# Kernel tuning notes

Hardware: AMD Instinct MI355X
Metric: run time of the kernel (lower is better)

Reference implementation:

```python
import jax, jax.numpy as jnp
import numpy as np

D_MODEL = 1024
EXPAND = 2
D_INNER = D_MODEL * EXPAND  # 2048 independent SSM channels
D_STATE = 16
BATCH = 4
SEQ = 4096


def setup_inputs() -> dict:
    key = jax.random.key(0)
    ks = jax.random.split(key, 10)
    w = lambda k, shape, scale=0.02: jax.random.normal(k, shape, jnp.float32) * scale
    return {
        "x": jax.random.normal(ks[0], (BATCH, SEQ, D_MODEL), jnp.float32),
        "w_in": w(ks[1], (D_MODEL, D_INNER)),
        "b_in": jnp.zeros((D_INNER,), jnp.float32),
        "w_gate": w(ks[2], (D_MODEL, D_INNER)),
        "b_gate": jnp.zeros((D_INNER,), jnp.float32),
        # per-channel linear SSM params: h_t = A h_{t-1} + B x_t ; y_t = C . h_t
        "A": w(ks[3], (D_INNER, D_STATE, D_STATE), 0.05),  # small spectral radius -> stable recurrence
        "B_ssm": w(ks[4], (D_INNER, D_STATE), 0.1),
        "C_ssm": w(ks[5], (D_INNER, D_STATE), 0.1),
        "w_out": w(ks[6], (D_INNER, D_MODEL)),
        "b_out": jnp.zeros((D_MODEL,), jnp.float32),
    }


def reference(x, w_in, b_in, w_gate, b_gate, A, B_ssm, C_ssm, w_out, b_out):
    # x: [B, S, D]
    x_proj = x @ w_in + b_in                     # [B, S, C]
    gate = jax.nn.sigmoid(x @ w_gate + b_gate)   # [B, S, C]

    def step(h, xt):
        # h: [B, C, N] state for all channels; xt: [B, C] scalar input per channel
        h = jnp.einsum("cnm,bcm->bcn", A, h) + B_ssm[None] * xt[:, :, None]
        y = jnp.einsum("bcn,cn->bc", h, C_ssm)
        return h, y

    h0 = jnp.zeros((x.shape[0], D_INNER, D_STATE), x.dtype)
    xs = jnp.swapaxes(x_proj, 0, 1)              # [S, B, C]
    _, ys = jax.lax.scan(step, h0, xs)           # ys: [S, B, C]
    ssm_out = jnp.swapaxes(ys, 0, 1)             # [B, S, C]

    y = ssm_out * gate
    return y @ w_out + b_out                     # [B, S, D]
```

## Files before the change

kernel.cpp:

```cpp
#include <hip/hip_runtime.h>
#include <hip/hip_bf16.h>

#define D_MODEL 1024
#define D_INNER 2048
#define D_STATE 16
#define BATCH   4
#define SEQ     4096
#define MROWS   (BATCH * SEQ)

#define LTAPS 16
#define TSPAN 64

using bf16 = __hip_bfloat16;

typedef __attribute__((ext_vector_type(8))) short bf16x8;
typedef __attribute__((ext_vector_type(4))) float f32x4;

__device__ __forceinline__ float bf2f(bf16 v) { return __bfloat162float(v); }
__device__ __forceinline__ unsigned short f2bfbits(float f) {
  bf16 h = __float2bfloat16(f);
  return *(unsigned short*)&h;
}

#define AS1CAST(p) ((const __attribute__((address_space(1))) unsigned int*)(unsigned long long)(p))
#define AS3CAST(p) ((__attribute__((address_space(3))) unsigned int*)(unsigned long long)(p))

#define FENCE() asm volatile("" ::: "memory")
#define BAR() do { FENCE(); __builtin_amdgcn_s_barrier(); FENCE(); } while (0)
#define WAIT_LGKM0() asm volatile("s_waitcnt lgkmcnt(0)" ::: "memory")

#define TILE_E (256 * 64)

struct G8 {
  const bf16 *gA, *gB;
  size_t K64, K128;
  int stageLds;
  int baseA0, baseA1;
  int baseB0, baseB1;
  int wr, wc, lane;
};

__device__ __forceinline__ void g8_setup(G8& g, const bf16* A, const bf16* BT,
                                         int m0, int n0, int K)
{
  const int tid = threadIdx.x;
  g.lane = tid & 63;
  const int wv = tid >> 6;
  g.wr = wv >> 2;
  g.wc = wv & 3;
  const int lr = g.lane >> 3, sl = g.lane & 7;
  g.gA = A  + (size_t)(m0 + wv * 8 + lr) * K + (sl ^ lr) * 8;
  g.gB = BT + (size_t)(n0 + wv * 8 + lr) * K + (sl ^ lr) * 8;
  g.K64  = (size_t)64 * K;
  g.K128 = (size_t)128 * K;
  g.stageLds = wv * 8 * 64;
  const int fla = g.lane & 15, cb = g.lane >> 4;
  const int s0 = cb ^ (fla & 7), s1 = s0 ^ 4;
  g.baseA0 = (g.wr * 64 + fla) * 64 + s0 * 8;
  g.baseA1 = (g.wr * 64 + fla) * 64 + s1 * 8;
  g.baseB0 = (g.wc * 32 + fla) * 64 + s0 * 8;
  g.baseB1 = (g.wc * 32 + fla) * 64 + s1 * 8;
}

__device__ __forceinline__ void g8_stageA(const G8& g, bf16* dstTile, int h, int tau)
{
  const bf16* s = g.gA + (h ? g.K128 : (size_t)0) + (size_t)tau * 64;
  bf16* d = dstTile + g.stageLds + h * (128 * 64);
  __builtin_amdgcn_global_load_lds(AS1CAST(s), AS3CAST(d), 16, 0, 0);
  __builtin_amdgcn_global_load_lds(AS1CAST(s + g.K64), AS3CAST(d + 64 * 64), 16, 0, 0);
}

__device__ __forceinline__ void g8_stageB(const G8& g, bf16* dstTile, int h, int tau)
{
  const bf16* s = g.gB + (h ? g.K128 : (size_t)0) + (size_t)tau * 64;
  bf16* d = dstTile + g.stageLds + h * (128 * 64);
  __builtin_amdgcn_global_load_lds(AS1CAST(s), AS3CAST(d), 16, 0, 0);
  __builtin_amdgcn_global_load_lds(AS1CAST(s + g.K64), AS3CAST(d + 64 * 64), 16, 0, 0);
}

#define LOAD_A(MH) do { _Pragma("unroll") \
  for (int mi = 0; mi < 4; ++mi) { \
    af[mi][0] = *(const bf16x8*)&At[g.baseA0 + (MH) * 8192 + mi * 1024]; \
    af[mi][1] = *(const bf16x8*)&At[g.baseA1 + (MH) * 8192 + mi * 1024]; \
  } } while (0)

#define LOAD_B(NH) do { _Pragma("unroll") \
  for (int ni = 0; ni < 2; ++ni) { \
    bfr[ni][0] = *(const bf16x8*)&Bt[g.baseB0 + (NH) * 8192 + ni * 1024]; \
    bfr[ni][1] = *(const bf16x8*)&Bt[g.baseB1 + (NH) * 8192 + ni * 1024]; \
  } } while (0)

#define MFMA_Q(MH, NH) do { _Pragma("unroll") \
  for (int mi = 0; mi < 4; ++mi) { _Pragma("unroll") \
    for (int ni = 0; ni < 2; ++ni) { \
      acc[MH][NH][mi][ni] = __builtin_amdgcn_mfma_f32_16x16x32_bf16( \
          af[mi][0], bfr[ni][0], acc[MH][NH][mi][ni], 0, 0, 0); \
      acc[MH][NH][mi][ni] = __builtin_amdgcn_mfma_f32_16x16x32_bf16( \
          af[mi][1], bfr[ni][1], acc[MH][NH][mi][ni], 0, 0, 0); \
    } } } while (0)

__device__ __forceinline__ void g8_main(const G8& g, bf16* As, bf16* Bs,
                                        f32x4 (&acc)[2][2][4][2], int K)
{
  const int nt = K >> 6;
  bf16* A0 = As;  bf16* A1 = As + TILE_E;
  bf16* B0 = Bs;  bf16* B1 = Bs + TILE_E;

  g8_stageA(g, A0, 0, 0);
  g8_stageB(g, B0, 1, 0);
  g8_stageA(g, A0, 1, 0);
  g8_stageB(g, B0, 0, 0);
  if (nt > 1) {
    g8_stageA(g, A1, 0, 1);
    g8_stageB(g, B1, 1, 1);
    g8_stageA(g, A1, 1, 1);
    asm volatile("s_waitcnt vmcnt(6)" ::: "memory");
  } else {
    asm volatile("s_waitcnt vmcnt(0)" ::: "memory");
  }
  BAR();

  bf16x8 af[4][2], bfr[2][2];

  for (int t = 0; t < nt; ++t) {
    const bf16* At = (t & 1) ? A1 : A0;
    const bf16* Bt = (t & 1) ? B1 : B0;
    bf16* Asame = (t & 1) ? A1 : A0;
    bf16* Bsame = (t & 1) ? B1 : B0;
    bf16* Bnext = (t & 1) ? B0 : B1;

    LOAD_A(0); LOAD_B(0);
    if (t + 1 < nt) g8_stageB(g, Bnext, 0, t + 1);
    asm volatile("s_waitcnt lgkmcnt(8)" ::: "memory");
    BAR();
    WAIT_LGKM0();
    __builtin_amdgcn_s_setprio(1);
    MFMA_Q(0, 0);
    __builtin_amdgcn_s_setprio(0);
    BAR();

    LOAD_B(1);
    if (t + 2 < nt) g8_stageA(g, Asame, 0, t + 2);
    BAR();
    WAIT_LGKM0();
    __builtin_amdgcn_s_setprio(1);
    MFMA_Q(0, 1);
    __builtin_amdgcn_s_setprio(0);
    BAR();

    LOAD_A(1);
    if (t + 2 < nt) g8_stageB(g, Bsame, 1, t + 2);
    BAR();
    WAIT_LGKM0();
    __builtin_amdgcn_s_setprio(1);
    MFMA_Q(1, 1);
    __builtin_amdgcn_s_setprio(0);
    BAR();

    LOAD_B(0);
    if (t + 2 < nt) g8_stageA(g, Asame, 1, t + 2);
    if (t < nt - 2) asm volatile("s_waitcnt vmcnt(6)" ::: "memory");
    else            asm volatile("s_waitcnt vmcnt(0)" ::: "memory");
    BAR();
    WAIT_LGKM0();
    __builtin_amdgcn_s_setprio(1);
    MFMA_Q(1, 0);
    __builtin_amdgcn_s_setprio(0);
    BAR();
  }
}

__global__ __launch_bounds__(512, 2) void gemm_proj_dual(
    const bf16* __restrict__ A,
    const bf16* __restrict__ BT,
    const float* __restrict__ bias_in, const float* __restrict__ bias_gate,
    bf16* __restrict__ xp, bf16* __restrict__ gate)
{
  __shared__ alignas(16) bf16 As[2 * TILE_E];
  __shared__ alignas(16) bf16 Bs[2 * TILE_E];

  const int b = blockIdx.x;
  const int swz = (b & 7) * 128 + (b >> 3);
  const int bm = swz >> 4, bn = swz & 15;
  const int m0 = bm * 256, n0 = bn * 256;

  G8 g;
  g8_setup(g, A, BT, m0, n0, D_MODEL);

  f32x4 acc[2][2][4][2];
#pragma unroll
  for (int a1 = 0; a1 < 2; ++a1)
#pragma unroll
    for (int a2 = 0; a2 < 2; ++a2)
#pragma unroll
      for (int a3 = 0; a3 < 4; ++a3)
#pragma unroll
        for (int a4 = 0; a4 < 2; ++a4)
          acc[a1][a2][a3][a4] = (f32x4){0.f, 0.f, 0.f, 0.f};

  g8_main(g, As, Bs, acc, D_MODEL);

  const bool isGate = (n0 >= D_INNER);
  const int  nloc0  = n0 - (isGate ? D_INNER : 0);
  const float* bias = isGate ? bias_gate : bias_in;
  bf16* dst         = isGate ? gate : xp;

  const int crow = (g.lane >> 4) * 4;
  const int ccol = g.lane & 15;
#pragma unroll
  for (int mh = 0; mh < 2; ++mh)
#pragma unroll
    for (int nh = 0; nh < 2; ++nh)
#pragma unroll
      for (int mi = 0; mi < 4; ++mi)
#pragma unroll
        for (int ni = 0; ni < 2; ++ni) {
          const int col = nloc0 + nh * 128 + g.wc * 32 + ni * 16 + ccol;
          const float bcol = bias[col];
#pragma unroll
          for (int r = 0; r < 4; ++r) {
            const size_t row = (size_t)(m0 + mh * 128 + g.wr * 64 + mi * 16 + crow + r);
            float v = acc[mh][nh][mi][ni][r] + bcol;
            if (isGate) v = 1.0f / (1.0f + __expf(-v));
            dst[row * D_INNER + col] = __float2bfloat16(v);
          }
        }
}

__global__ __launch_bounds__(512, 2) void gemm_out(
    const bf16* __restrict__ A,
    const bf16* __restrict__ BT,
    const float* __restrict__ bias,
    float* __restrict__ C)
{
  __shared__ alignas(16) bf16 As[2 * TILE_E];
  __shared__ alignas(16) bf16 Bs[2 * TILE_E];

  const int b = blockIdx.x;
  const int swz = (b & 7) * 32 + (b >> 3);
  const int bm = swz >> 2, bn = swz & 3;
  const int m0 = bm * 256, n0 = bn * 256;

  G8 g;
  g8_setup(g, A, BT, m0, n0, D_INNER);

  f32x4 acc[2][2][4][2];
#pragma unroll
  for (int a1 = 0; a1 < 2; ++a1)
#pragma unroll
    for (int a2 = 0; a2 < 2; ++a2)
#pragma unroll
      for (int a3 = 0; a3 < 4; ++a3)
#pragma unroll
        for (int a4 = 0; a4 < 2; ++a4)
          acc[a1][a2][a3][a4] = (f32x4){0.f, 0.f, 0.f, 0.f};

  g8_main(g, As, Bs, acc, D_INNER);

  const int crow = (g.lane >> 4) * 4;
  const int ccol = g.lane & 15;
#pragma unroll
  for (int mh = 0; mh < 2; ++mh)
#pragma unroll
    for (int nh = 0; nh < 2; ++nh)
#pragma unroll
      for (int mi = 0; mi < 4; ++mi)
#pragma unroll
        for (int ni = 0; ni < 2; ++ni) {
          const int col = n0 + nh * 128 + g.wc * 32 + ni * 16 + ccol;
          const float bcol = bias[col];
#pragma unroll
          for (int r = 0; r < 4; ++r) {
            const size_t row = (size_t)(m0 + mh * 128 + g.wr * 64 + mi * 16 + crow + r);
            C[row * D_MODEL + col] = acc[mh][nh][mi][ni][r] + bcol;
          }
        }
}

__global__ __launch_bounds__(256) void f32_to_bf16(
    const float* __restrict__ in, bf16* __restrict__ out, int n4)
{
  const int i = (blockIdx.x * 256 + threadIdx.x);
  if (i >= n4) return;
  const float4 v = *(const float4*)(in + (size_t)i * 4);
  ushort4 r;
  r.x = f2bfbits(v.x); r.y = f2bfbits(v.y); r.z = f2bfbits(v.z); r.w = f2bfbits(v.w);
  *(ushort4*)(out + (size_t)i * 4) = r;
}

__global__ __launch_bounds__(256) void transpose_to_bf16(
    const float* __restrict__ in, bf16* __restrict__ out, int R, int C)
{
  __shared__ float tile[32][33];
  const int c0 = blockIdx.x * 32, r0 = blockIdx.y * 32;
  const int tx = threadIdx.x & 31, ty = threadIdx.x >> 5;
#pragma unroll
  for (int i = ty; i < 32; i += 8)
    tile[i][tx] = in[(size_t)(r0 + i) * C + c0 + tx];
  __syncthreads();
#pragma unroll
  for (int i = ty; i < 32; i += 8)
    out[(size_t)(c0 + i) * R + r0 + tx] = __float2bfloat16(tile[tx][i]);
}

__device__ __forceinline__ float4 load4f(const float* p) { return *(const float4*)p; }

__global__ __launch_bounds__(256) void ssm_taps(
    const float* __restrict__ A, const float* __restrict__ Bv,
    const float* __restrict__ Cv, float* __restrict__ g)
{
  const int c = blockIdx.x * blockDim.x + threadIdx.x;
  if (c >= D_INNER) return;
  const float* Ac = A + (size_t)c * D_STATE * D_STATE;
  float v[D_STATE], cr[D_STATE];
#pragma unroll
  for (int i = 0; i < D_STATE; ++i) {
    v[i]  = Bv[(size_t)c * D_STATE + i];
    cr[i] = Cv[(size_t)c * D_STATE + i];
  }
  for (int m = 0; m < LTAPS; ++m) {
    float y = 0.f;
#pragma unroll
    for (int i = 0; i < D_STATE; ++i) y += cr[i] * v[i];
    g[(size_t)m * D_INNER + c] = y;
    float nv[D_STATE];
#pragma unroll
    for (int n = 0; n < D_STATE; ++n) {
      const float4 a0 = load4f(Ac + n * D_STATE + 0);
      const float4 a1 = load4f(Ac + n * D_STATE + 4);
      const float4 a2 = load4f(Ac + n * D_STATE + 8);
      const float4 a3 = load4f(Ac + n * D_STATE + 12);
      float s = a0.x * v[0] + a0.y * v[1] + a0.z * v[2] + a0.w * v[3];
      s += a1.x * v[4] + a1.y * v[5] + a1.z * v[6] + a1.w * v[7];
      s += a2.x * v[8] + a2.y * v[9] + a2.z * v[10] + a2.w * v[11];
      s += a3.x * v[12] + a3.y * v[13] + a3.z * v[14] + a3.w * v[15];
      nv[n] = s;
    }
#pragma unroll
    for (int i = 0; i < D_STATE; ++i) v[i] = nv[i];
  }
}

__global__ __launch_bounds__(256) void conv_gate(
    const bf16* __restrict__ xp, bf16* __restrict__ gate_io,
    const float* __restrict__ g)
{
  const int c  = blockIdx.x * blockDim.x + threadIdx.x;
  const int b  = blockIdx.z;
  const int t0 = blockIdx.y * TSPAN;

  float gg[LTAPS];
#pragma unroll
  for (int m = 0; m < LTAPS; ++m) gg[m] = g[(size_t)m * D_INNER + c];

  const size_t baseBC = ((size_t)b * SEQ) * D_INNER + c;

  float w[2 * LTAPS];
#pragma unroll
  for (int j = 0; j < LTAPS; ++j) {
    const int t = t0 - LTAPS + j;
    w[j] = (t >= 0) ? bf2f(xp[baseBC + (size_t)t * D_INNER]) : 0.f;
  }

  for (int blk = 0; blk < TSPAN; blk += LTAPS) {
#pragma unroll
    for (int j = 0; j < LTAPS; ++j)
      w[LTAPS + j] = bf2f(xp[baseBC + (size_t)(t0 + blk + j) * D_INNER]);
#pragma unroll
    for (int j = 0; j < LTAPS; ++j) {
      float y = 0.f;
#pragma unroll
      for (int m = 0; m < LTAPS; ++m) y += gg[m] * w[LTAPS + j - m];
      const size_t idx = baseBC + (size_t)(t0 + blk + j) * D_INNER;
      const float gt = bf2f(gate_io[idx]);
      gate_io[idx] = __float2bfloat16(y * gt);
    }
#pragma unroll
    for (int j = 0; j < LTAPS; ++j) w[j] = w[j + LTAPS];
  }
}

extern "C" void kernel_launch(void* const* d_in, const int* in_sizes, int n_in,
                              void* d_out, int out_size, void* d_ws, size_t ws_size,
                              hipStream_t stream)
{
  const float* x      = (const float*)d_in[0];
  const float* w_in   = (const float*)d_in[1];
  const float* b_in   = (const float*)d_in[2];
  const float* w_gate = (const float*)d_in[3];
  const float* b_gate = (const float*)d_in[4];
  const float* A      = (const float*)d_in[5];
  const float* B_ssm  = (const float*)d_in[6];
  const float* C_ssm  = (const float*)d_in[7];
  const float* w_out  = (const float*)d_in[8];
  const float* b_out  = (const float*)d_in[9];
  float* out = (float*)d_out;

  char* ws = (char*)d_ws;
  bf16*  gate  = (bf16*)(ws);
  bf16*  xbf   = (bf16*)(ws + 67108864);
  bf16*  wcatT = (bf16*)(ws + 100663296);
  bf16*  w_otT = (bf16*)(ws + 109051904);
  float* taps  = (float*)(ws + 113246208);
  bf16*  xp    = (bf16*)d_out;

  dim3 blk(256);

  hipLaunchKernelGGL(ssm_taps, dim3(D_INNER / 256), blk, 0, stream, A, B_ssm, C_ssm, taps);
  hipLaunchKernelGGL(f32_to_bf16, dim3((MROWS * D_MODEL / 4) / 256), blk, 0, stream,
                     x, xbf, MROWS * D_MODEL / 4);
  hipLaunchKernelGGL(transpose_to_bf16, dim3(D_INNER / 32, D_MODEL / 32), blk, 0, stream,
                     w_in, wcatT, D_MODEL, D_INNER);
  hipLaunchKernelGGL(transpose_to_bf16, dim3(D_INNER / 32, D_MODEL / 32), blk, 0, stream,
                     w_gate, wcatT + (size_t)D_INNER * D_MODEL, D_MODEL, D_INNER);
  hipLaunchKernelGGL(transpose_to_bf16, dim3(D_MODEL / 32, D_INNER / 32), blk, 0, stream,
                     w_out, w_otT, D_INNER, D_MODEL);

  dim3 gblk(512);
  hipLaunchKernelGGL(gemm_proj_dual, dim3((2 * D_INNER / 256) * (MROWS / 256)), gblk, 0, stream,
                     xbf, wcatT, b_in, b_gate, xp, gate);

  dim3 gc(D_INNER / 256, SEQ / TSPAN, BATCH);
  hipLaunchKernelGGL(conv_gate, gc, blk, 0, stream, xp, gate, taps);

  hipLaunchKernelGGL(gemm_out, dim3((D_MODEL / 256) * (MROWS / 256)), gblk, 0, stream,
                     gate, w_otT, b_out, out);
}
```

Before: 408.3 us.

## Restructure GEMM main loop software pipeline and vectorize conv_gate over channel pairs

The GEMM K-loop is rewritten as a templated per-tile routine. It interleaves LDS fragment reads, next-tile global-to-LDS staging and MFMA quarters, and uses one vmcnt wait plus a single barrier per tile in place of several barriers per quarter. Fragments for the next tile are preloaded at the end of each tile, and the prologue now stages only one tile ahead instead of two. Separately, conv_gate processes two adjacent channels per thread with 32-bit loads and stores, halving the grid to cut memory instructions. The new GEMM schedule reduces sync overhead, but the shallower prefetch may expose global load latency and raises register pressure.

New measurement: 391.0 us. -4.2%, faster.

```diff
diff --git a/kernel.cpp b/kernel.cpp
--- a/kernel.cpp
+++ b/kernel.cpp
@@ -21,13 +21,17 @@
   bf16 h = __float2bfloat16(f);
   return *(unsigned short*)&h;
 }
+__device__ __forceinline__ float bfbits2f(unsigned short u) {
+  union { float f; unsigned int i; } x; x.i = (unsigned int)u << 16; return x.f;
+}
 
 #define AS1CAST(p) ((const __attribute__((address_space(1))) unsigned int*)(unsigned long long)(p))
 #define AS3CAST(p) ((__attribute__((address_space(3))) unsigned int*)(unsigned long long)(p))
 
 #define FENCE() asm volatile("" ::: "memory")
 #define BAR() do { FENCE(); __builtin_amdgcn_s_barrier(); FENCE(); } while (0)
-#define WAIT_LGKM0() asm volatile("s_waitcnt lgkmcnt(0)" ::: "memory")
+#define PRIO1 __builtin_amdgcn_s_setprio(1)
+#define PRIO0 __builtin_amdgcn_s_setprio(0)
 
 #define TILE_E (256 * 64)
 
@@ -78,96 +82,89 @@
   __builtin_amdgcn_global_load_lds(AS1CAST(s + g.K64), AS3CAST(d + 64 * 64), 16, 0, 0);
 }
 
-#define LOAD_A(MH) do { _Pragma("unroll") \
-  for (int mi = 0; mi < 4; ++mi) { \
-    af[mi][0] = *(const bf16x8*)&At[g.baseA0 + (MH) * 8192 + mi * 1024]; \
-    af[mi][1] = *(const bf16x8*)&At[g.baseA1 + (MH) * 8192 + mi * 1024]; \
+__device__ __forceinline__ void rdA(bf16x8 (&d)[4], const bf16* T, int base, int mh)
+{
+#pragma unroll
+  for (int mi = 0; mi < 4; ++mi)
+    d[mi] = *(const bf16x8*)&T[base + mh * 8192 + mi * 1024];
+}
+__device__ __forceinline__ void rdB(bf16x8 (&d)[2], const bf16* T, int base, int nh)
+{
+#pragma unroll
+  for (int ni = 0; ni < 2; ++ni)
+    d[ni] = *(const bf16x8*)&T[base + nh * 8192 + ni * 1024];
+}
+
+#define MQS(MH, NH, AF, BF) do { _Pragma("unroll") \
+  for (int mi = 0; mi < 4; ++mi) { _Pragma("unroll") \
+    for (int ni = 0; ni < 2; ++ni) \
+      acc[MH][NH][mi][ni] = __builtin_amdgcn_mfma_f32_16x16x32_bf16( \
+          (AF)[mi], (BF)[ni], acc[MH][NH][mi][ni], 0, 0, 0); \
   } } while (0)
 
-#define LOAD_B(NH) do { _Pragma("unroll") \
-  for (int ni = 0; ni < 2; ++ni) { \
-    bfr[ni][0] = *(const bf16x8*)&Bt[g.baseB0 + (NH) * 8192 + ni * 1024]; \
-    bfr[ni][1] = *(const bf16x8*)&Bt[g.baseB1 + (NH) * 8192 + ni * 1024]; \
-  } } while (0)
-
-#define MFMA_Q(MH, NH) do { _Pragma("unroll") \
-  for (int mi = 0; mi < 4; ++mi) { _Pragma("unroll") \
-    for (int ni = 0; ni < 2; ++ni) { \
-      acc[MH][NH][mi][ni] = __builtin_amdgcn_mfma_f32_16x16x32_bf16( \
-          af[mi][0], bfr[ni][0], acc[MH][NH][mi][ni], 0, 0, 0); \
-      acc[MH][NH][mi][ni] = __builtin_amdgcn_mfma_f32_16x16x32_bf16( \
-          af[mi][1], bfr[ni][1], acc[MH][NH][mi][ni], 0, 0, 0); \
-    } } } while (0)
+template<bool MORE>
+__device__ __forceinline__ void g8_tile(const G8& g, const bf16* At, const bf16* Bt,
+    bf16* An, bf16* Bn, int t, f32x4 (&acc)[2][2][4][2],
+    bf16x8 (&aP)[4], bf16x8 (&aQ)[4], bf16x8 (&b0s0)[2], bf16x8 (&b0s1)[2],
+    bf16x8 (&b1s0)[2], bf16x8 (&b1s1)[2])
+{
+  rdA(aQ, At, g.baseA1, 0);
+  if constexpr (MORE) g8_stageA(g, An, 0, t + 1);
+  PRIO1; MQS(0, 0, aP, b0s0); PRIO0;
+  rdB(b1s0, Bt, g.baseB0, 1);
+  if constexpr (MORE) g8_stageB(g, Bn, 0, t + 1);
+  PRIO1; MQS(0, 0, aQ, b0s1); PRIO0;
+  rdB(b1s1, Bt, g.baseB1, 1);
+  if constexpr (MORE) g8_stageA(g, An, 1, t + 1);
+  PRIO1; MQS(0, 1, aP, b1s0); PRIO0;
+  rdA(aP, At, g.baseA0, 1);
+  if constexpr (MORE) g8_stageB(g, Bn, 1, t + 1);
+  PRIO1; MQS(0, 1, aQ, b1s1); PRIO0;
+  rdA(aQ, At, g.baseA1, 1);
+  PRIO1; MQS(1, 1, aP, b1s0); PRIO0;
+  PRIO1; MQS(1, 1, aQ, b1s1); PRIO0;
+  PRIO1; MQS(1, 0, aP, b0s0); PRIO0;
+  if constexpr (MORE) {
+    asm volatile("s_waitcnt vmcnt(0)" ::: "memory");
+    BAR();
+  }
+  PRIO1; MQS(1, 0, aQ, b0s1); PRIO0;
+  if constexpr (MORE) {
+    rdA(aP, An, g.baseA0, 0);
+    rdB(b0s0, Bn, g.baseB0, 0);
+    rdB(b0s1, Bn, g.baseB1, 0);
+  }
+}
 
 __device__ __forceinline__ void g8_main(const G8& g, bf16* As, bf16* Bs,
                                         f32x4 (&acc)[2][2][4][2], int K)
 {
   const int nt = K >> 6;
-  bf16* A0 = As;  bf16* A1 = As + TILE_E;
-  bf16* B0 = Bs;  bf16* B1 = Bs + TILE_E;
+  bf16* A0 = As; bf16* A1 = As + TILE_E;
+  bf16* B0 = Bs; bf16* B1 = Bs + TILE_E;
 
   g8_stageA(g, A0, 0, 0);
+  g8_stageB(g, B0, 0, 0);
+  g8_stageA(g, A0, 1, 0);
   g8_stageB(g, B0, 1, 0);
-  g8_stageA(g, A0, 1, 0);
-  g8_stageB(g, B0, 0, 0);
-  if (nt > 1) {
-    g8_stageA(g, A1, 0, 1);
-    g8_stageB(g, B1, 1, 1);
-    g8_stageA(g, A1, 1, 1);
-    asm volatile("s_waitcnt vmcnt(6)" ::: "memory");
-  } else {
-    asm volatile("s_waitcnt vmcnt(0)" ::: "memory");
-  }
+  asm volatile("s_waitcnt vmcnt(0)" ::: "memory");
   BAR();
 
-  bf16x8 af[4][2], bfr[2][2];
-
-  for (int t = 0; t < nt; ++t) {
-    const bf16* At = (t & 1) ? A1 : A0;
-    const bf16* Bt = (t & 1) ? B1 : B0;
-    bf16* Asame = (t & 1) ? A1 : A0;
-    bf16* Bsame = (t & 1) ? B1 : B0;
-    bf16* Bnext = (t & 1) ? B0 : B1;
-
-    LOAD_A(0); LOAD_B(0);
-    if (t + 1 < nt) g8_stageB(g, Bnext, 0, t + 1);
-    asm volatile("s_waitcnt lgkmcnt(8)" ::: "memory");
-    BAR();
-    WAIT_LGKM0();
-    __builtin_amdgcn_s_setprio(1);
-    MFMA_Q(0, 0);
-    __builtin_amdgcn_s_setprio(0);
-    BAR();
-
-    LOAD_B(1);
-    if (t + 2 < nt) g8_stageA(g, Asame, 0, t + 2);
-    BAR();
-    WAIT_LGKM0();
-    __builtin_amdgcn_s_setprio(1);
-    MFMA_Q(0, 1);
-    __builtin_amdgcn_s_setprio(0);
-    BAR();
-
-    LOAD_A(1);
-    if (t + 2 < nt) g8_stageB(g, Bsame, 1, t + 2);
-    BAR();
-    WAIT_LGKM0();
-    __builtin_amdgcn_s_setprio(1);
-    MFMA_Q(1, 1);
-    __builtin_amdgcn_s_setprio(0);
-    BAR();
-
-    LOAD_B(0);
-    if (t + 2 < nt) g8_stageA(g, Asame, 1, t + 2);
-    if (t < nt - 2) asm volatile("s_waitcnt vmcnt(6)" ::: "memory");
-    else            asm volatile("s_waitcnt vmcnt(0)" ::: "memory");
-    BAR();
-    WAIT_LGKM0();
-    __builtin_amdgcn_s_setprio(1);
-    MFMA_Q(1, 0);
-    __builtin_amdgcn_s_setprio(0);
-    BAR();
-  }
+  bf16x8 aP[4], aQ[4], b0s0[2], b0s1[2], b1s0[2], b1s1[2];
+  rdA(aP, A0, g.baseA0, 0);
+  rdB(b0s0, B0, g.baseB0, 0);
+  rdB(b0s1, B0, g.baseB1, 0);
+
+  for (int t = 0; t < nt - 1; ++t) {
+    bf16* At = (t & 1) ? A1 : A0;
+    bf16* Bt = (t & 1) ? B1 : B0;
+    bf16* An = (t & 1) ? A0 : A1;
+    bf16* Bn = (t & 1) ? B0 : B1;
+    g8_tile<true>(g, At, Bt, An, Bn, t, acc, aP, aQ, b0s0, b0s1, b1s0, b1s1);
+  }
+  bf16* At = ((nt - 1) & 1) ? A1 : A0;
+  bf16* Bt = ((nt - 1) & 1) ? B1 : B0;
+  g8_tile<false>(g, At, Bt, At, Bt, nt - 1, acc, aP, aQ, b0s0, b0s1, b1s0, b1s1);
 }
 
 __global__ __launch_bounds__(512, 2) void gemm_proj_dual(
@@ -345,38 +342,54 @@
     const bf16* __restrict__ xp, bf16* __restrict__ gate_io,
     const float* __restrict__ g)
 {
-  const int c  = blockIdx.x * blockDim.x + threadIdx.x;
+  const int cp = blockIdx.x * blockDim.x + threadIdx.x;
+  const int c  = cp * 2;
   const int b  = blockIdx.z;
   const int t0 = blockIdx.y * TSPAN;
 
-  float gg[LTAPS];
-#pragma unroll
-  for (int m = 0; m < LTAPS; ++m) gg[m] = g[(size_t)m * D_INNER + c];
+  float gg0[LTAPS], gg1[LTAPS];
+#pragma unroll
+  for (int m = 0; m < LTAPS; ++m) {
+    gg0[m] = g[(size_t)m * D_INNER + c];
+    gg1[m] = g[(size_t)m * D_INNER + c + 1];
+  }
 
   const size_t baseBC = ((size_t)b * SEQ) * D_INNER + c;
 
-  float w[2 * LTAPS];
+  float w0[2 * LTAPS], w1[2 * LTAPS];
 #pragma unroll
   for (int j = 0; j < LTAPS; ++j) {
     const int t = t0 - LTAPS + j;
-    w[j] = (t >= 0) ? bf2f(xp[baseBC + (size_t)t * D_INNER]) : 0.f;
+    if (t >= 0) {
+      const ushort2 v = *(const ushort2*)&xp[baseBC + (size_t)t * D_INNER];
+      w0[j] = bfbits2f(v.x); w1[j] = bfbits2f(v.y);
+    } else { w0[j] = 0.f; w1[j] = 0.f; }
   }
 
   for (int blk = 0; blk < TSPAN; blk += LTAPS) {
 #pragma unroll
-    for (int j = 0; j < LTAPS; ++j)
-      w[LTAPS + j] = bf2f(xp[baseBC + (size_t)(t0 + blk + j) * D_INNER]);
-#pragma unroll
     for (int j = 0; j < LTAPS; ++j) {
-      float y = 0.f;
-#pragma unroll
-      for (int m = 0; m < LTAPS; ++m) y += gg[m] * w[LTAPS + j - m];
+      const ushort2 v = *(const ushort2*)&xp[baseBC + (size_t)(t0 + blk + j) * D_INNER];
+      w0[LTAPS + j] = bfbits2f(v.x); w1[LTAPS + j] = bfbits2f(v.y);
+    }
+#pragma unroll
+    for (int j = 0; j < LTAPS; ++j) {
+      float y0 = 0.f, y1 = 0.f;
+#pragma unroll
+      for (int m = 0; m < LTAPS; ++m) {
+        y0 += gg0[m] * w0[LTAPS + j - m];
+        y1 += gg1[m] * w1[LTAPS + j - m];
+      }
       const size_t idx = baseBC + (size_t)(t0 + blk + j) * D_INNER;
-      const float gt = bf2f(gate_io[idx]);
-      gate_io[idx] = __float2bfloat16(y * gt);
+      const unsigned int gv = *(const unsigned int*)&gate_io[idx];
+      const float g0 = bfbits2f((unsigned short)(gv & 0xffffu));
+      const float g1 = bfbits2f((unsigned short)(gv >> 16));
+      const unsigned int ov =
+          (unsigned int)f2bfbits(y0 * g0) | ((unsigned int)f2bfbits(y1 * g1) << 16);
+      *(unsigned int*)&gate_io[idx] = ov;
     }
 #pragma unroll
-    for (int j = 0; j < LTAPS; ++j) w[j] = w[j + LTAPS];
+    for (int j = 0; j < LTAPS; ++j) { w0[j] = w0[j + LTAPS]; w1[j] = w1[j + LTAPS]; }
   }
 }
 
@@ -420,7 +433,7 @@
   hipLaunchKernelGGL(gemm_proj_dual, dim3((2 * D_INNER / 256) * (MROWS / 256)), gblk, 0, stream,
                      xbf, wcatT, b_in, b_gate, xp, gate);
 
-  dim3 gc(D_INNER / 256, SEQ / TSPAN, BATCH);
+  dim3 gc(D_INNER / 2 / 256, SEQ / TSPAN, BATCH);
   hipLaunchKernelGGL(conv_gate, gc, blk, 0, stream, xp, gate, taps);
 
   hipLaunchKernelGGL(gemm_out, dim3((D_MODEL / 256) * (MROWS / 256)), gblk, 0, stream,
```
